# Kernel tuning notes

Measured on AMD Instinct MI355X. Metric: run time of the kernel, lower is better.

Reference implementation:

```python
import jax, jax.numpy as jnp
import numpy as np
from jax import lax

B_, L_, D_ = 4, 2048, 256
DI, NS, DC, DTR = 512, 16, 4, 16  # d_inner=2*D, d_state, d_conv, dt_rank=ceil(D/16)
DFF = 4 * D_


def setup_inputs():
    key = jax.random.key(0)
    ks = jax.random.split(key, 20)
    rn = lambda k, s, sc=0.02: jax.random.normal(k, s, jnp.float32) * sc
    return {
        "x": jax.random.normal(ks[0], (B_, L_, D_), jnp.float32),
        "in_proj_w": rn(ks[1], (2 * DI, D_)), "in_proj_b": jnp.zeros((2 * DI,), jnp.float32),
        "conv_w": rn(ks[2], (DI, DC), 0.1), "conv_b": jnp.zeros((DI,), jnp.float32),
        "x_proj_w": rn(ks[3], (DTR + 2 * NS, DI)),
        "dt_proj_w": rn(ks[4], (DI, DTR), 0.1), "dt_proj_b": rn(ks[5], (DI,), 0.5),
        "A_log": jnp.log(jnp.tile(jnp.arange(1, NS + 1, dtype=jnp.float32), (DI, 1))),
        "D_ssm": jnp.ones((DI,), jnp.float32),
        "out_proj_w": rn(ks[6], (D_, DI)), "out_proj_b": jnp.zeros((D_,), jnp.float32),
        "ln1_g": jnp.ones((D_,), jnp.float32), "ln1_b": jnp.zeros((D_,), jnp.float32),
        "fc1_w": rn(ks[7], (DFF, D_)), "fc1_b": jnp.zeros((DFF,), jnp.float32),
        "fc2_w": rn(ks[8], (D_, DFF)), "fc2_b": jnp.zeros((D_,), jnp.float32),
        "ln2_g": jnp.ones((D_,), jnp.float32), "ln2_b": jnp.zeros((D_,), jnp.float32),
    }


def _layer_norm(x, g, b, eps=1e-5):
    m = jnp.mean(x, -1, keepdims=True)
    v = jnp.mean((x - m) ** 2, -1, keepdims=True)
    return (x - m) / jnp.sqrt(v + eps) * g + b


def _mamba(x, in_proj_w, in_proj_b, conv_w, conv_b, x_proj_w, dt_proj_w, dt_proj_b, A_log, D_ssm, out_proj_w, out_proj_b):
    B, L, D = x.shape
    xz = x @ in_proj_w.T + in_proj_b                       # [B,L,2*DI]
    xi, z = jnp.split(xz, 2, axis=-1)
    # causal depthwise conv over time
    xc = jnp.transpose(xi, (0, 2, 1))                       # [B,DI,L]
    xc = lax.conv_general_dilated(xc, conv_w[:, None, :], (1,), [(DC - 1, 0)],
                                  dimension_numbers=("NCH", "OIH", "NCH"),
                                  feature_group_count=DI)
    xi = jax.nn.silu(jnp.transpose(xc + conv_b[None, :, None], (0, 2, 1)))  # [B,L,DI]
    x_dbl = xi @ x_proj_w.T                                 # [B,L,DTR+2*NS]
    dt, Bs, Cs = jnp.split(x_dbl, [DTR, DTR + NS], axis=-1)
    dt = jax.nn.softplus(dt @ dt_proj_w.T + dt_proj_b)      # [B,L,DI]
    A = -jnp.exp(A_log)                                     # [DI,NS]
    dA = jnp.exp(dt[..., None] * A)                         # [B,L,DI,NS]
    dBu = dt[..., None] * Bs[:, :, None, :] * xi[..., None]  # [B,L,DI,NS]
    dA_t = jnp.moveaxis(dA, 1, 0)
    dBu_t = jnp.moveaxis(dBu, 1, 0)
    C_t = jnp.moveaxis(Cs, 1, 0)                            # [L,B,NS]

    def step(h, inp):
        a, bu, c = inp
        h = a * h + bu                                      # [B,DI,NS]
        y = jnp.einsum("bdn,bn->bd", h, c)
        return h, y

    h0 = jnp.zeros((B, DI, NS), x.dtype)
    _, ys = lax.scan(step, h0, (dA_t, dBu_t, C_t))
    y = jnp.moveaxis(ys, 0, 1) + xi * D_ssm                 # [B,L,DI]
    y = y * jax.nn.silu(z)
    return y @ out_proj_w.T + out_proj_b


def reference(x, in_proj_w, in_proj_b, conv_w, conv_b, x_proj_w, dt_proj_w, dt_proj_b,
              A_log, D_ssm, out_proj_w, out_proj_b, ln1_g, ln1_b, fc1_w, fc1_b,
              fc2_w, fc2_b, ln2_g, ln2_b):
    gelu = lambda t: jax.nn.gelu(t, approximate=False)
    ssm = _mamba(x, in_proj_w, in_proj_b, conv_w, conv_b, x_proj_w, dt_proj_w,
                 dt_proj_b, A_log, D_ssm, out_proj_w, out_proj_b)
    y = _layer_norm(x + ssm, ln1_g, ln1_b)                  # dropout = identity (eval)
    ffn = gelu(gelu(y @ fc1_w.T + fc1_b) @ fc2_w.T + fc2_b)
    return _layer_norm(y + ffn, ln2_g, ln2_b)
```

## Files before the change

### kernel.cpp

```cpp
#include <hip/hip_runtime.h>

typedef __bf16 bf16x8 __attribute__((ext_vector_type(8)));
typedef float  f32x4  __attribute__((ext_vector_type(4)));

#define AS1 __attribute__((address_space(1)))
#define AS3 __attribute__((address_space(3)))

__device__ __forceinline__ float bf2f(ushort u) {
    union { unsigned int i; float f; } v; v.i = ((unsigned int)u) << 16; return v.f;
}
__device__ __forceinline__ ushort f2bf(float f) {
    union { float f; unsigned int i; } v; v.f = f;
    unsigned int i = v.i;
    unsigned int r = i + 0x7FFFu + ((i >> 16) & 1u);
    return (ushort)(r >> 16);
}
__device__ __forceinline__ float bflo(unsigned int u) { return bf2f((ushort)(u & 0xFFFFu)); }
__device__ __forceinline__ float bfhi(unsigned int u) { return bf2f((ushort)(u >> 16)); }
__device__ __forceinline__ float gelu_f(float v) {
    return 0.5f * v * (1.f + erff(v * 0.70710678118654752f));
}

__device__ __forceinline__ bool sniff_inline(const ushort* __restrict__ x) {
    const int lane = threadIdx.x & 63;
    int cnt = 0;
    #pragma unroll
    for (int r = 0; r < 4; r++) {
        const ushort u = x[lane + r * 64];
        const int e = (u >> 7) & 0xFF;
        if ((u & 0x7FFF) == 0 || (e >= 112 && e <= 141)) cnt++;
    }
    #pragma unroll
    for (int o = 32; o > 0; o >>= 1) cnt += __shfl_xor(cnt, o);
    return cnt >= 224;
}

struct CanonArgs {
    const void* src[20];
    int off[20];
    int total;
};

__launch_bounds__(256)
__global__ void canon_k(CanonArgs a, ushort* __restrict__ dst, ushort* __restrict__ xpw_pad,
                        const ushort* __restrict__ sniffx)
{
    const int i = blockIdx.x * 256 + threadIdx.x;
    if (i >= a.total) {
        const int j = i - a.total;
        if (j < 8192) xpw_pad[24576 + j] = 0;
        return;
    }
    const bool fl = sniff_inline(sniffx);
    int s = 0;
    #pragma unroll
    for (int t = 1; t < 20; t++) if (i >= a.off[t]) s = t;
    const int li = i - a.off[s];
    ushort v;
    if (fl) v = ((const ushort*)a.src[s])[li];
    else    v = f2bf(((const float*)a.src[s])[li]);
    dst[i] = v;
    if (s == 5) xpw_pad[li] = v;
}

template<int BM, int BN, int EPI, bool OUTF>
__launch_bounds__(256, 4)
__global__ void gemm_bt(const ushort* __restrict__ A, int lda, const ushort* __restrict__ W,
                        const ushort* __restrict__ bias, const ushort* __restrict__ resid,
                        void* __restrict__ Cb, int N, int K)
{
    constexpr int WMT = BM / 32;
    constexpr int WNT = BN / 32;
    __shared__ __align__(16) ushort As[BM * 32];
    __shared__ __align__(16) ushort Bs[BN * 32];
    const int tid  = threadIdx.x;
    const int wave = tid >> 6;
    const int lane = tid & 63;
    const int m0 = blockIdx.x * BM;
    const int n0 = blockIdx.y * BN;
    const int wm = (wave >> 1) * (BM / 2);
    const int wn = (wave & 1) * (BN / 2);
    const int lrow = lane & 15;
    const int quad = lane >> 4;

    f32x4 acc[WMT][WNT];
    #pragma unroll
    for (int i = 0; i < WMT; i++)
        #pragma unroll
        for (int j = 0; j < WNT; j++)
            #pragma unroll
            for (int r = 0; r < 4; r++) acc[i][j][r] = 0.f;

    for (int k0 = 0; k0 < K; k0 += 32) {
        #pragma unroll
        for (int t = 0; t < BM / 64; t++) {
            const int inst = t * 4 + wave;
            const int row  = inst * 16 + (lane >> 2);
            const int sub  = lane & 3;
            const ushort* gp = A + (size_t)(m0 + row) * lda + (k0 + sub * 8);
            __builtin_amdgcn_global_load_lds((AS1 void*)(void*)gp,
                                             (AS3 void*)(As + inst * 512), 16, 0, 0);
        }
        #pragma unroll
        for (int t = 0; t < BN / 64; t++) {
            const int inst = t * 4 + wave;
            const int row  = inst * 16 + (lane >> 2);
            const int sub  = lane & 3;
            const ushort* gp = W + (size_t)(n0 + row) * K + (k0 + sub * 8);
            __builtin_amdgcn_global_load_lds((AS1 void*)(void*)gp,
                                             (AS3 void*)(Bs + inst * 512), 16, 0, 0);
        }
        __syncthreads();
        bf16x8 afr[WMT], bfr[WNT];
        #pragma unroll
        for (int i = 0; i < WMT; i++)
            afr[i] = *(const bf16x8*)&As[(wm + i * 16 + lrow) * 32 + quad * 8];
        #pragma unroll
        for (int j = 0; j < WNT; j++)
            bfr[j] = *(const bf16x8*)&Bs[(wn + j * 16 + lrow) * 32 + quad * 8];
        #pragma unroll
        for (int i = 0; i < WMT; i++)
            #pragma unroll
            for (int j = 0; j < WNT; j++)
                acc[i][j] = __builtin_amdgcn_mfma_f32_16x16x32_bf16(afr[i], bfr[j], acc[i][j], 0, 0, 0);
        __syncthreads();
    }

    #pragma unroll
    for (int i = 0; i < WMT; i++) {
        const int gm = m0 + wm + i * 16 + quad * 4;
        #pragma unroll
        for (int j = 0; j < WNT; j++) {
            const int gn = n0 + wn + j * 16 + lrow;
            const float bv = bf2f(bias[gn]);
            #pragma unroll
            for (int r = 0; r < 4; r++) {
                float v = acc[i][j][r] + bv;
                if (EPI == 1) v = gelu_f(v);
                if (EPI == 2) v += bf2f(resid[(size_t)(gm + r) * N + gn]);
                if (OUTF) ((float*)Cb)[(size_t)(gm + r) * N + gn] = v;
                else      ((ushort*)Cb)[(size_t)(gm + r) * N + gn] = f2bf(v);
            }
        }
    }
}

__launch_bounds__(512)
__global__ void ln1_k(float* __restrict__ y1pre, const ushort* __restrict__ g1,
                      const ushort* __restrict__ b1, ushort* __restrict__ y1b)
{
    const int tid  = threadIdx.x;
    const int wave = tid >> 6;
    const int lane = tid & 63;
    const int row  = blockIdx.x * 8 + wave;
    const int col0 = lane * 4;

    const f32x4 a = *(const f32x4*)&y1pre[(size_t)row * 256 + col0];
    float S = 0.f, Q = 0.f;
    #pragma unroll
    for (int k = 0; k < 4; k++) { S += a[k]; Q += a[k] * a[k]; }
    #pragma unroll
    for (int o = 32; o > 0; o >>= 1) {
        S += __shfl_xor(S, o);
        Q += __shfl_xor(Q, o);
    }
    const float mean = S * (1.f / 256.f);
    const float var  = Q * (1.f / 256.f) - mean * mean;
    const float rs   = rsqrtf(var + 1e-5f);

    float of[4];
    ushort ob[4];
    #pragma unroll
    for (int k = 0; k < 4; k++) {
        of[k] = (a[k] - mean) * rs * bf2f(g1[col0 + k]) + bf2f(b1[col0 + k]);
        ob[k] = f2bf(of[k]);
    }
    *(f32x4*)&y1pre[(size_t)row * 256 + col0] = *(f32x4*)&of[0];
    *(ushort4*)&y1b[(size_t)row * 256 + col0] = *(ushort4*)&ob[0];
}

__launch_bounds__(512)
__global__ void convx_k(const ushort* __restrict__ xz, const ushort* __restrict__ cw,
                        const ushort* __restrict__ cb, const ushort* __restrict__ xpw_pad,
                        ushort* __restrict__ xc, float* __restrict__ xdbl)
{
    __shared__ __align__(16) ushort xcs[16 * 520];
    const int tid  = threadIdx.x;
    const int wave = tid >> 6;
    const int lane = tid & 63;
    const int lrow = lane & 15;
    const int quad = lane >> 4;
    const int c = blockIdx.x, b = blockIdx.y;
    const int t0 = b * 2048 + c * 16;

    {
        const int d8 = (tid & 63) * 8;
        ushort wl[32];
        *(uint4*)&wl[0]  = *(const uint4*)&cw[d8 * 4];
        *(uint4*)&wl[8]  = *(const uint4*)&cw[d8 * 4 + 8];
        *(uint4*)&wl[16] = *(const uint4*)&cw[d8 * 4 + 16];
        *(uint4*)&wl[24] = *(const uint4*)&cw[d8 * 4 + 24];
        ushort bl[8];
        *(uint4*)&bl[0] = *(const uint4*)&cb[d8];
        #pragma unroll
        for (int it = 0; it < 2; it++) {
            const int trow = it * 8 + wave;
            const int t = t0 + trow;
            const int l = t & 2047;
            float acc[8];
            #pragma unroll
            for (int j = 0; j < 8; j++) acc[j] = bf2f(bl[j]);
            #pragma unroll
            for (int k = 0; k < 4; k++) {
                const int ls = l - 3 + k;
                if (ls >= 0) {
                    ushort xl[8];
                    *(uint4*)&xl[0] = *(const uint4*)&xz[(size_t)(t - 3 + k) * 1024 + d8];
                    #pragma unroll
                    for (int j = 0; j < 8; j++) acc[j] += bf2f(xl[j]) * bf2f(wl[j * 4 + k]);
                }
            }
            ushort ol[8];
            #pragma unroll
            for (int j = 0; j < 8; j++) {
                const float s = acc[j] / (1.f + __expf(-acc[j]));
                ol[j] = f2bf(s);
            }
            *(uint4*)&xcs[trow * 520 + d8] = *(uint4*)&ol[0];
        }
    }
    __syncthreads();

    if (wave < 3) {
        const int nt = wave;
        const ushort* bptr = xpw_pad + (size_t)(nt * 16 + lrow) * 512 + quad * 8;
        f32x4 acc = {0.f, 0.f, 0.f, 0.f};
        #pragma unroll
        for (int hh = 0; hh < 2; hh++) {
            bf16x8 Bv[8];
            #pragma unroll
            for (int s = 0; s < 8; s++)
                Bv[s] = *(const bf16x8*)(bptr + hh * 256 + s * 32);
            #pragma unroll
            for (int s = 0; s < 8; s++) {
                const bf16x8 afr = *(const bf16x8*)&xcs[lrow * 520 + hh * 256 + s * 32 + quad * 8];
                acc = __builtin_amdgcn_mfma_f32_16x16x32_bf16(afr, Bv[s], acc, 0, 0, 0);
            }
        }
        const int col = nt * 16 + lrow;
        if (col < 48) {
            #pragma unroll
            for (int r = 0; r < 4; r++)
                xdbl[(size_t)(t0 + quad * 4 + r) * 64 + col] = acc[r];
        }
    }

    {
        const int row = tid >> 5;
        const int col = (tid & 31) * 16;
        *(uint4*)&xc[(size_t)(t0 + row) * 512 + col]     = *(const uint4*)&xcs[row * 520 + col];
        *(uint4*)&xc[(size_t)(t0 + row) * 512 + col + 8] = *(const uint4*)&xcs[row * 520 + col + 8];
    }
}

__launch_bounds__(256)
__global__ void scan1_k(const ushort* __restrict__ xc, const float* __restrict__ xdbl,
                        const ushort* __restrict__ dtw, const ushort* __restrict__ dtb,
                        const ushort* __restrict__ Alog,
                        float* __restrict__ summh, float* __restrict__ sdtb)
{
    __shared__ float XD[16 * 48];
    const int tid = threadIdx.x;
    const int c = blockIdx.x, dh = blockIdx.y, b = blockIdx.z;
    const int t0 = b * 2048 + c * 16;
    const int d = dh * 256 + tid;

    for (int e = tid; e < 768; e += 256)
        XD[e] = xdbl[(size_t)(t0 + (e / 48)) * 64 + (e % 48)];
    __syncthreads();

    const uint4 w0 = *(const uint4*)&dtw[d * 16];
    const uint4 w1 = *(const uint4*)&dtw[d * 16 + 8];
    const float wd[16] = { bflo(w0.x), bfhi(w0.x), bflo(w0.y), bfhi(w0.y),
                           bflo(w0.z), bfhi(w0.z), bflo(w0.w), bfhi(w0.w),
                           bflo(w1.x), bfhi(w1.x), bflo(w1.y), bfhi(w1.y),
                           bflo(w1.z), bfhi(w1.z), bflo(w1.w), bfhi(w1.w) };
    const uint4 a0 = *(const uint4*)&Alog[d * 16];
    const uint4 a1 = *(const uint4*)&Alog[d * 16 + 8];
    const float al[16] = { bflo(a0.x), bfhi(a0.x), bflo(a0.y), bfhi(a0.y),
                           bflo(a0.z), bfhi(a0.z), bflo(a0.w), bfhi(a0.w),
                           bflo(a1.x), bfhi(a1.x), bflo(a1.y), bfhi(a1.y),
                           bflo(a1.z), bfhi(a1.z), bflo(a1.w), bfhi(a1.w) };
    const float dtbv = bf2f(dtb[d]);
    float A[16], h[16];
    #pragma unroll
    for (int n = 0; n < 16; n++) { A[n] = -__expf(al[n]); h[n] = 0.f; }
    float sdt = 0.f;
    for (int i = 0; i < 16; i++) {
        const float* Xr = &XD[i * 48];
        float s0 = dtbv, s1 = 0.f, s2 = 0.f, s3 = 0.f;
        #pragma unroll
        for (int k = 0; k < 16; k += 4) {
            s0 += Xr[k]     * wd[k];
            s1 += Xr[k + 1] * wd[k + 1];
            s2 += Xr[k + 2] * wd[k + 2];
            s3 += Xr[k + 3] * wd[k + 3];
        }
        const float s = (s0 + s1) + (s2 + s3);
        const float dtv = (s > 15.f) ? s : __logf(1.f + __expf(s));
        const float xiv = bf2f(xc[(size_t)(t0 + i) * 512 + d]);
        const float dx = dtv * xiv;
        sdt += dtv;
        #pragma unroll
        for (int n = 0; n < 16; n++) {
            const float da = __expf(dtv * A[n]);
            h[n] = da * h[n] + dx * Xr[16 + n];
        }
    }
    const size_t bh = ((size_t)(b * 128 + c) * 16) * 512 + d;
    #pragma unroll
    for (int n = 0; n < 16; n++) summh[bh + (size_t)n * 512] = h[n];
    sdtb[(size_t)(b * 128 + c) * 512 + d] = sdt;
}

__launch_bounds__(128)
__global__ void combine_k(float* __restrict__ summh, const float* __restrict__ sdtb,
                          const ushort* __restrict__ Alog)
{
    const int b  = blockIdx.x >> 6;
    const int n  = (blockIdx.x >> 2) & 15;
    const int dq = blockIdx.x & 3;
    const int d  = dq * 128 + threadIdx.x;
    const float An = -__expf(bf2f(Alog[d * 16 + n]));
    float h = 0.f;
    #pragma unroll
    for (int q = 0; q < 4; q++) {
        float p[32], hl[32], ho[32];
        #pragma unroll
        for (int c2 = 0; c2 < 32; c2++) {
            const int cc = q * 32 + c2;
            hl[c2] = summh[((size_t)(b * 128 + cc) * 16 + n) * 512 + d];
            p[c2]  = __expf(An * sdtb[(size_t)(b * 128 + cc) * 512 + d]);
        }
        #pragma unroll
        for (int c2 = 0; c2 < 32; c2++) {
            ho[c2] = h;
            h = p[c2] * h + hl[c2];
        }
        #pragma unroll
        for (int c2 = 0; c2 < 32; c2++)
            summh[((size_t)(b * 128 + (q * 32 + c2)) * 16 + n) * 512 + d] = ho[c2];
    }
}

__launch_bounds__(256)
__global__ void scan2_k(const ushort* __restrict__ xz, ushort* __restrict__ xc,
                        const float* __restrict__ xdbl,
                        const ushort* __restrict__ dtw, const ushort* __restrict__ dtb,
                        const ushort* __restrict__ Alog, const float* __restrict__ summh,
                        const ushort* __restrict__ Dssm)
{
    __shared__ float XD[16 * 48];
    const int tid = threadIdx.x;
    const int c = blockIdx.x, dh = blockIdx.y, b = blockIdx.z;
    const int t0 = b * 2048 + c * 16;
    const int d = dh * 256 + tid;

    for (int e = tid; e < 768; e += 256)
        XD[e] = xdbl[(size_t)(t0 + (e / 48)) * 64 + (e % 48)];
    __syncthreads();

    const uint4 w0 = *(const uint4*)&dtw[d * 16];
    const uint4 w1 = *(const uint4*)&dtw[d * 16 + 8];
    const float wd[16] = { bflo(w0.x), bfhi(w0.x), bflo(w0.y), bfhi(w0.y),
                           bflo(w0.z), bfhi(w0.z), bflo(w0.w), bfhi(w0.w),
                           bflo(w1.x), bfhi(w1.x), bflo(w1.y), bfhi(w1.y),
                           bflo(w1.z), bfhi(w1.z), bflo(w1.w), bfhi(w1.w) };
    const uint4 a0 = *(const uint4*)&Alog[d * 16];
    const uint4 a1 = *(const uint4*)&Alog[d * 16 + 8];
    const float al[16] = { bflo(a0.x), bfhi(a0.x), bflo(a0.y), bfhi(a0.y),
                           bflo(a0.z), bfhi(a0.z), bflo(a0.w), bfhi(a0.w),
                           bflo(a1.x), bfhi(a1.x), bflo(a1.y), bfhi(a1.y),
                           bflo(a1.z), bfhi(a1.z), bflo(a1.w), bfhi(a1.w) };
    const float dtbv = bf2f(dtb[d]);
    float A[16], h[16];
    #pragma unroll
    for (int n = 0; n < 16; n++) A[n] = -__expf(al[n]);
    const size_t bh = ((size_t)(b * 128 + c) * 16) * 512 + d;
    #pragma unroll
    for (int n = 0; n < 16; n++) h[n] = summh[bh + (size_t)n * 512];
    const float Dv = bf2f(Dssm[d]);

    for (int i = 0; i < 16; i++) {
        const int t = t0 + i;
        const float* Xr = &XD[i * 48];
        float s0 = dtbv, s1 = 0.f, s2 = 0.f, s3 = 0.f;
        #pragma unroll
        for (int k = 0; k < 16; k += 4) {
            s0 += Xr[k]     * wd[k];
            s1 += Xr[k + 1] * wd[k + 1];
            s2 += Xr[k + 2] * wd[k + 2];
            s3 += Xr[k + 3] * wd[k + 3];
        }
        const float s = (s0 + s1) + (s2 + s3);
        const float dtv = (s > 15.f) ? s : __logf(1.f + __expf(s));
        const float xiv = bf2f(xc[(size_t)t * 512 + d]);
        const float dx = dtv * xiv;
        float yv0 = 0.f, yv1 = 0.f;
        #pragma unroll
        for (int n = 0; n < 16; n += 2) {
            const float da0 = __expf(dtv * A[n]);
            const float da1 = __expf(dtv * A[n + 1]);
            h[n]     = da0 * h[n]     + dx * Xr[16 + n];
            h[n + 1] = da1 * h[n + 1] + dx * Xr[17 + n];
            yv0 += h[n]     * Xr[32 + n];
            yv1 += h[n + 1] * Xr[33 + n];
        }
        float yv = yv0 + yv1;
        yv += xiv * Dv;
        const float zv = bf2f(xz[(size_t)t * 1024 + 512 + d]);
        yv *= zv / (1.f + __expf(-zv));
        xc[(size_t)t * 512 + d] = f2bf(yv);
    }
}

__launch_bounds__(512)
__global__ void ln2_k(const float* __restrict__ y2, const float* __restrict__ y1f,
                      const ushort* __restrict__ g2, const ushort* __restrict__ b2,
                      void* __restrict__ dout, const ushort* __restrict__ sniffx)
{
    const int tid  = threadIdx.x;
    const int wave = tid >> 6;
    const int lane = tid & 63;
    const int row  = blockIdx.x * 8 + wave;
    const int col0 = lane * 4;

    const f32x4 a = *(const f32x4*)&y2[(size_t)row * 256 + col0];
    const f32x4 rsd = *(const f32x4*)&y1f[(size_t)row * 256 + col0];
    float v[4];
    float S = 0.f, Q = 0.f;
    #pragma unroll
    for (int k = 0; k < 4; k++) {
        v[k] = gelu_f(a[k]) + rsd[k];
        S += v[k];
        Q += v[k] * v[k];
    }
    #pragma unroll
    for (int o = 32; o > 0; o >>= 1) {
        S += __shfl_xor(S, o);
        Q += __shfl_xor(Q, o);
    }
    const float mean = S * (1.f / 256.f);
    const float var  = Q * (1.f / 256.f) - mean * mean;
    const float rs   = rsqrtf(var + 1e-5f);

    const bool fl = sniff_inline(sniffx);
    if (fl) {
        ushort o4[4];
        #pragma unroll
        for (int k = 0; k < 4; k++)
            o4[k] = f2bf((v[k] - mean) * rs * bf2f(g2[col0 + k]) + bf2f(b2[col0 + k]));
        *(ushort4*)((ushort*)dout + (size_t)row * 256 + col0) = *(ushort4*)&o4[0];
    } else {
        float o4[4];
        #pragma unroll
        for (int k = 0; k < 4; k++)
            o4[k] = (v[k] - mean) * rs * bf2f(g2[col0 + k]) + bf2f(b2[col0 + k]);
        *(float4*)((float*)dout + (size_t)row * 256 + col0) = *(float4*)&o4[0];
    }
}

extern "C" void kernel_launch(void* const* d_in, const int* in_sizes, int n_in,
                              void* d_out, int out_size, void* d_ws, size_t ws_size,
                              hipStream_t stream)
{
    char* ws = (char*)d_ws;
    ushort* canon = (ushort*)(ws + 256);

    static const int coff[20] = {
        0,        2097152,  2359296,  2360320,  2362368,
        2362880,  2387456,  2395648,  2396160,  2404352,
        2404864,  2535936,  2536192,  2536448,  2536704,
        2798848,  2799872,  3062016,  3062272,  3062528 };
    static const int ctot = 3062784;

    CanonArgs ca;
    for (int i = 0; i < 20; i++) { ca.src[i] = d_in[i]; ca.off[i] = coff[i]; }
    ca.total = ctot;

    const ushort* cx   = canon + coff[0];
    const ushort* cipw = canon + coff[1];
    const ushort* cipb = canon + coff[2];
    const ushort* ccw  = canon + coff[3];
    const ushort* ccb  = canon + coff[4];
    const ushort* cdtw = canon + coff[6];
    const ushort* cdtb = canon + coff[7];
    const ushort* calog= canon + coff[8];
    const ushort* cdssm= canon + coff[9];
    const ushort* copw = canon + coff[10];
    const ushort* copb = canon + coff[11];
    const ushort* cln1g= canon + coff[12];
    const ushort* cln1b= canon + coff[13];
    const ushort* cf1w = canon + coff[14];
    const ushort* cf1b = canon + coff[15];
    const ushort* cf2w = canon + coff[16];
    const ushort* cf2b = canon + coff[17];
    const ushort* cln2g= canon + coff[18];
    const ushort* cln2b= canon + coff[19];

    ushort* xpw_pad = (ushort*)(ws + 6291456);
    ushort* xz      = (ushort*)(ws + 8388608);
    float*  y1pre   = (float*)(ws + 8388608);
    ushort* y1b     = (ushort*)(ws + 16777216);
    float*  xdbl    = (float*)(ws + 25165824);
    float*  summh   = (float*)(ws + 27262976);
    ushort* h1      = (ushort*)(ws + 27262976);
    float*  sdtb    = (float*)(ws + 44040192);
    ushort* xc      = (ushort*)(ws + 45088768);
    float*  y2      = (float*)(ws + 45088768);
    const ushort* sx = (const ushort*)d_in[0];

    canon_k<<<(ctot + 8192 + 255) / 256, 256, 0, stream>>>(ca, canon, xpw_pad, sx);
    gemm_bt<64, 128, 0, false><<<dim3(128, 8), 256, 0, stream>>>(
        cx, 256, cipw, cipb, nullptr, xz, 1024, 256);
    convx_k<<<dim3(128, 4), 512, 0, stream>>>(xz, ccw, ccb, xpw_pad, xc, xdbl);
    scan1_k<<<dim3(128, 2, 4), 256, 0, stream>>>(xc, xdbl, cdtw, cdtb, calog, summh, sdtb);
    combine_k<<<256, 128, 0, stream>>>(summh, sdtb, calog);
    scan2_k<<<dim3(128, 2, 4), 256, 0, stream>>>(xz, xc, xdbl, cdtw, cdtb, calog, summh, cdssm);
    gemm_bt<64, 64, 2, true><<<dim3(128, 4), 256, 0, stream>>>(
        xc, 512, copw, copb, cx, y1pre, 256, 512);
    ln1_k<<<1024, 512, 0, stream>>>(y1pre, cln1g, cln1b, y1b);
    gemm_bt<64, 128, 1, false><<<dim3(128, 8), 256, 0, stream>>>(
        y1b, 256, cf1w, cf1b, nullptr, h1, 1024, 256);
    gemm_bt<64, 64, 0, true><<<dim3(128, 4), 256, 0, stream>>>(
        h1, 1024, cf2w, cf2b, nullptr, y2, 256, 1024);
    ln2_k<<<1024, 512, 0, stream>>>(y2, y1pre, cln2g, cln2b, d_out, sx);
}
```

Measured before the change: 237.7 us.

## Fuse chunked scan passes into one cooperative kernel with grid syncs

```diff
diff --git a/kernel.cpp b/kernel.cpp
--- a/kernel.cpp
+++ b/kernel.cpp
@@ -1,4 +1,7 @@
 #include <hip/hip_runtime.h>
+#include <hip/hip_cooperative_groups.h>
+
+namespace cg = cooperative_groups;
 
 typedef __bf16 bf16x8 __attribute__((ext_vector_type(8)));
 typedef float  f32x4  __attribute__((ext_vector_type(4)));
@@ -260,6 +263,127 @@
         const int col = (tid & 31) * 16;
         *(uint4*)&xc[(size_t)(t0 + row) * 512 + col]     = *(const uint4*)&xcs[row * 520 + col];
         *(uint4*)&xc[(size_t)(t0 + row) * 512 + col + 8] = *(const uint4*)&xcs[row * 520 + col + 8];
+    }
+}
+
+__launch_bounds__(256, 4)
+__global__ void scanfused_k(const ushort* __restrict__ xz, ushort* __restrict__ xc,
+                            const float* __restrict__ xdbl,
+                            const ushort* __restrict__ dtw, const ushort* __restrict__ dtb,
+                            const ushort* __restrict__ Alog, const ushort* __restrict__ Dssm,
+                            float* __restrict__ summh, float* __restrict__ sdtb)
+{
+    cg::grid_group grid = cg::this_grid();
+    __shared__ float XD[16 * 48];
+    const int tid = threadIdx.x;
+    const int c = blockIdx.x, dh = blockIdx.y, b = blockIdx.z;
+    const int t0 = b * 2048 + c * 16;
+    const int d = dh * 256 + tid;
+
+    for (int e = tid; e < 768; e += 256)
+        XD[e] = xdbl[(size_t)(t0 + (e / 48)) * 64 + (e % 48)];
+    __syncthreads();
+
+    const uint4 a0 = *(const uint4*)&Alog[d * 16];
+    const uint4 a1 = *(const uint4*)&Alog[d * 16 + 8];
+    float A[16] = { -__expf(bflo(a0.x)), -__expf(bfhi(a0.x)), -__expf(bflo(a0.y)), -__expf(bfhi(a0.y)),
+                    -__expf(bflo(a0.z)), -__expf(bfhi(a0.z)), -__expf(bflo(a0.w)), -__expf(bfhi(a0.w)),
+                    -__expf(bflo(a1.x)), -__expf(bfhi(a1.x)), -__expf(bflo(a1.y)), -__expf(bfhi(a1.y)),
+                    -__expf(bflo(a1.z)), -__expf(bfhi(a1.z)), -__expf(bflo(a1.w)), -__expf(bfhi(a1.w)) };
+
+    float dtv_r[16], h[16];
+    #pragma unroll
+    for (int n = 0; n < 16; n++) h[n] = 0.f;
+    float sdt = 0.f;
+    {
+        const uint4 w0 = *(const uint4*)&dtw[d * 16];
+        const uint4 w1 = *(const uint4*)&dtw[d * 16 + 8];
+        const float wd[16] = { bflo(w0.x), bfhi(w0.x), bflo(w0.y), bfhi(w0.y),
+                               bflo(w0.z), bfhi(w0.z), bflo(w0.w), bfhi(w0.w),
+                               bflo(w1.x), bfhi(w1.x), bflo(w1.y), bfhi(w1.y),
+                               bflo(w1.z), bfhi(w1.z), bflo(w1.w), bfhi(w1.w) };
+        const float dtbv = bf2f(dtb[d]);
+        #pragma unroll
+        for (int i = 0; i < 16; i++) {
+            const float* Xr = &XD[i * 48];
+            float s0 = dtbv, s1 = 0.f, s2 = 0.f, s3 = 0.f;
+            #pragma unroll
+            for (int k = 0; k < 16; k += 4) {
+                s0 += Xr[k]     * wd[k];
+                s1 += Xr[k + 1] * wd[k + 1];
+                s2 += Xr[k + 2] * wd[k + 2];
+                s3 += Xr[k + 3] * wd[k + 3];
+            }
+            const float s = (s0 + s1) + (s2 + s3);
+            const float dtv = (s > 15.f) ? s : __logf(1.f + __expf(s));
+            dtv_r[i] = dtv;
+            const float dx = dtv * bf2f(xc[(size_t)(t0 + i) * 512 + d]);
+            sdt += dtv;
+            #pragma unroll
+            for (int n = 0; n < 16; n++)
+                h[n] = __expf(dtv * A[n]) * h[n] + dx * Xr[16 + n];
+        }
+    }
+    const size_t bh = ((size_t)(b * 128 + c) * 16) * 512 + d;
+    #pragma unroll
+    for (int n = 0; n < 16; n++) summh[bh + (size_t)n * 512] = h[n];
+    sdtb[(size_t)(b * 128 + c) * 512 + d] = sdt;
+
+    grid.sync();
+
+    const int flat = blockIdx.x + 128 * (blockIdx.y + 2 * blockIdx.z);
+    if (flat < 256 && tid < 128) {
+        const int b2 = flat >> 6, n2 = (flat >> 2) & 15, dq = flat & 3;
+        const int d2 = dq * 128 + tid;
+        const float An = -__expf(bf2f(Alog[d2 * 16 + n2]));
+        float hp = 0.f;
+        #pragma unroll
+        for (int q = 0; q < 8; q++) {
+            float p[16], hl[16], ho[16];
+            #pragma unroll
+            for (int c2 = 0; c2 < 16; c2++) {
+                const int cc = q * 16 + c2;
+                hl[c2] = summh[((size_t)(b2 * 128 + cc) * 16 + n2) * 512 + d2];
+                p[c2]  = __expf(An * sdtb[(size_t)(b2 * 128 + cc) * 512 + d2]);
+            }
+            #pragma unroll
+            for (int c2 = 0; c2 < 16; c2++) {
+                ho[c2] = hp;
+                hp = p[c2] * hp + hl[c2];
+            }
+            #pragma unroll
+            for (int c2 = 0; c2 < 16; c2++)
+                summh[((size_t)(b2 * 128 + (q * 16 + c2)) * 16 + n2) * 512 + d2] = ho[c2];
+        }
+    }
+
+    grid.sync();
+
+    #pragma unroll
+    for (int n = 0; n < 16; n++) h[n] = summh[bh + (size_t)n * 512];
+    const float Dv = bf2f(Dssm[d]);
+    #pragma unroll
+    for (int i = 0; i < 16; i++) {
+        const int t = t0 + i;
+        const float* Xr = &XD[i * 48];
+        const float dtv = dtv_r[i];
+        const float xiv = bf2f(xc[(size_t)t * 512 + d]);
+        const float dx = dtv * xiv;
+        float yv0 = 0.f, yv1 = 0.f;
+        #pragma unroll
+        for (int n = 0; n < 16; n += 2) {
+            const float da0 = __expf(dtv * A[n]);
+            const float da1 = __expf(dtv * A[n + 1]);
+            h[n]     = da0 * h[n]     + dx * Xr[16 + n];
+            h[n + 1] = da1 * h[n + 1] + dx * Xr[17 + n];
+            yv0 += h[n]     * Xr[32 + n];
+            yv1 += h[n + 1] * Xr[33 + n];
+        }
+        float yv = yv0 + yv1;
+        yv += xiv * Dv;
+        const float zv = bf2f(xz[(size_t)t * 1024 + 512 + d]);
+        yv *= zv / (1.f + __expf(-zv));
+        xc[(size_t)t * 512 + d] = f2bf(yv);
     }
 }
 
@@ -524,9 +648,18 @@
     gemm_bt<64, 128, 0, false><<<dim3(128, 8), 256, 0, stream>>>(
         cx, 256, cipw, cipb, nullptr, xz, 1024, 256);
     convx_k<<<dim3(128, 4), 512, 0, stream>>>(xz, ccw, ccb, xpw_pad, xc, xdbl);
-    scan1_k<<<dim3(128, 2, 4), 256, 0, stream>>>(xc, xdbl, cdtw, cdtb, calog, summh, sdtb);
-    combine_k<<<256, 128, 0, stream>>>(summh, sdtb, calog);
-    scan2_k<<<dim3(128, 2, 4), 256, 0, stream>>>(xz, xc, xdbl, cdtw, cdtb, calog, summh, cdssm);
+    {
+        void* sargs[] = { (void*)&xz, (void*)&xc, (void*)&xdbl, (void*)&cdtw, (void*)&cdtb,
+                          (void*)&calog, (void*)&cdssm, (void*)&summh, (void*)&sdtb };
+        hipError_t ce = hipLaunchCooperativeKernel(
+            reinterpret_cast<void*>(&scanfused_k), dim3(128, 2, 4), dim3(256, 1, 1),
+            sargs, 0, stream);
+        if (ce != hipSuccess) {
+            scan1_k<<<dim3(128, 2, 4), 256, 0, stream>>>(xc, xdbl, cdtw, cdtb, calog, summh, sdtb);
+            combine_k<<<256, 128, 0, stream>>>(summh, sdtb, calog);
+            scan2_k<<<dim3(128, 2, 4), 256, 0, stream>>>(xz, xc, xdbl, cdtw, cdtb, calog, summh, cdssm);
+        }
+    }
     gemm_bt<64, 64, 2, true><<<dim3(128, 4), 256, 0, stream>>>(
         xc, 512, copw, copb, cx, y1pre, 256, 512);
     ln1_k<<<1024, 512, 0, stream>>>(y1pre, cln1g, cln1b, y1b);
```

Result: slower. 688.8 us (+189.7%).
